# Performance work log

Measured on AMD Instinct MI355X. Metric: run time of the kernel, lower is better.

The kernel has to match this reference:

```python
import jax, jax.numpy as jnp
import numpy as np

N_HEAD = 16
N_EMBD = 2048
HEAD_DIM = N_EMBD // N_HEAD


def setup_inputs() -> dict:
    key = jax.random.key(0)
    kx, kqkv, kp = jax.random.split(key, 3)
    B, S = 2, 2048
    x = jax.random.normal(kx, (B, S, N_EMBD), dtype=jnp.float32)
    # torch nn.Linear weights, stored as [out, in]; y = x @ W.T
    scale = 1.0 / np.sqrt(N_EMBD)
    Wqkv = jax.random.uniform(kqkv, (3 * N_EMBD, N_EMBD), dtype=jnp.float32, minval=-scale, maxval=scale)
    Wproj = jax.random.uniform(kp, (N_EMBD, N_EMBD), dtype=jnp.float32, minval=-scale, maxval=scale)
    return {"x": x, "Wqkv": Wqkv, "Wproj": Wproj}


def reference(x, Wqkv, Wproj):
    B, S, E = x.shape
    qkv = x @ Wqkv.T  # [B,S,3E]
    q, k, v = jnp.split(qkv, 3, axis=2)
    # [B,H,S,D]
    q = q.reshape(B, S, N_HEAD, HEAD_DIM).transpose(0, 2, 1, 3)
    k = k.reshape(B, S, N_HEAD, HEAD_DIM).transpose(0, 2, 1, 3)
    v = v.reshape(B, S, N_HEAD, HEAD_DIM).transpose(0, 2, 1, 3)
    scores = jnp.einsum('bhqd,bhkd->bhqk', q, k) / jnp.sqrt(jnp.float32(HEAD_DIM))
    causal = jnp.tril(jnp.ones((S, S), dtype=bool))  # [S,S]
    scores = jnp.where(causal[None, None, :, :], scores, -jnp.inf)
    weights = jax.nn.softmax(scores, axis=-1)
    out = jnp.einsum('bhqk,bhkd->bhqd', weights, v)  # [B,H,S,D]
    out = out.transpose(0, 2, 1, 3).reshape(B, S, E)
    return out @ Wproj.T
```

## Files before the change

kernel.cpp:

```cpp
#include <hip/hip_runtime.h>
#include <cstdint>
#include <cstddef>

typedef __bf16 bf16;
typedef __bf16 bf16x8 __attribute__((ext_vector_type(8)));
typedef float  f32x4  __attribute__((ext_vector_type(4)));

static_assert(sizeof(bf16x8) == 16, "bf16x8 must be 16B");

__device__ __forceinline__ void async_copy16(const bf16* g, bf16* l) {
  __builtin_amdgcn_global_load_lds(
      (__attribute__((address_space(1))) void*)(g),
      (__attribute__((address_space(3))) void*)(l),
      16, 0, 0);
}

__global__ __launch_bounds__(256)
void conv_f32_bf16(const float* __restrict__ s, bf16* __restrict__ d) {
  const size_t i = ((size_t)blockIdx.x * 256 + threadIdx.x) * 8;
  const f32x4 a = *(const f32x4*)(s + i);
  const f32x4 b = *(const f32x4*)(s + i + 4);
  bf16x8 o;
#pragma unroll
  for (int e = 0; e < 4; ++e) { o[e] = (bf16)a[e]; o[4 + e] = (bf16)b[e]; }
  *(bf16x8*)(d + i) = o;
}

template<int AMODE, int CMODE>
__global__ __launch_bounds__(256, 2)
void gemm_bt(const bf16* __restrict__ A, const bf16* __restrict__ W,
             float* __restrict__ Crow, bf16* __restrict__ Cq,
             bf16* __restrict__ Ck, bf16* __restrict__ Cvt,
             int M, int N, int K, int nbase) {
  __shared__ bf16 As[128 * 64];
  __shared__ bf16 Ws[128 * 64];

  const int tid  = threadIdx.x;
  const int wave = tid >> 6;
  const int lane = tid & 63;
  const int quad = lane >> 4;
  const int r    = lane & 15;
  const int m0 = blockIdx.y * 128;
  const int n0 = blockIdx.x * 128;
  const int wm = (wave >> 1) * 64;
  const int wn = (wave & 1) * 64;

  const int lrow   = lane >> 3;
  const int gchunk = (lane & 7) ^ lrow;

  f32x4 acc[4][4] = {};

  for (int k0 = 0; k0 < K; k0 += 64) {
    __syncthreads();
    for (int j = 0; j < 4; ++j) {
      const int rbase = (wave * 4 + j) * 8;
      const int rowA  = m0 + rbase + lrow;
      const bf16* aSrc;
      if constexpr (AMODE == 2) {
        const int b = rowA >> 11, s = rowA & 2047;
        aSrc = A + ((size_t)(b * 16 + (k0 >> 7)) * 2048 + s) * 128
                 + (k0 & 127) + gchunk * 8;
      } else {
        aSrc = A + (size_t)rowA * K + k0 + gchunk * 8;
      }
      async_copy16(aSrc, As + rbase * 64);
      async_copy16(W + (size_t)(n0 + rbase + lrow) * K + k0 + gchunk * 8,
                   Ws + rbase * 64);
    }
    __syncthreads();
    for (int ks = 0; ks < 2; ++ks) {
      bf16x8 af[4], bfv[4];
      for (int i = 0; i < 4; ++i) {
        const int ar = wm + i * 16 + r;
        af[i]  = *(const bf16x8*)(As + ar * 64 + (((ks * 4 + quad) ^ (ar & 7)) * 8));
        const int br = wn + i * 16 + r;
        bfv[i] = *(const bf16x8*)(Ws + br * 64 + (((ks * 4 + quad) ^ (br & 7)) * 8));
      }
      for (int i = 0; i < 4; ++i)
        for (int j = 0; j < 4; ++j)
          acc[i][j] = __builtin_amdgcn_mfma_f32_16x16x32_bf16(af[i], bfv[j], acc[i][j], 0, 0, 0);
    }
  }

  for (int i = 0; i < 4; ++i) {
    const int growb = m0 + wm + i * 16 + quad * 4;
    for (int j = 0; j < 4; ++j) {
      const int gcol = n0 + wn + j * 16 + r;
      for (int rg = 0; rg < 4; ++rg) {
        const int grow = growb + rg;
        if constexpr (CMODE == 1) {
          const int gc = nbase + gcol;
          const int which = gc >> 11;
          const int h = (gc >> 7) & 15;
          const int d = gc & 127;
          const int b = grow >> 11;
          const int s = grow & 2047;
          const bf16 v = (bf16)acc[i][j][rg];
          if (which == 0)
            Cq[(((size_t)b * 16 + h) * 2048 + s) * 128 + d] = v;
          else if (which == 1)
            Ck[(((size_t)b * 16 + h) * 2048 + s) * 128 + d] = v;
          else
            Cvt[(((size_t)b * 16 + h) * 128 + d) * 2048 + s] = v;
        } else {
          Crow[(size_t)grow * N + gcol] = acc[i][j][rg];
        }
      }
    }
  }
}

__global__ __launch_bounds__(256, 2)
void attn_kernel(bf16* __restrict__ Q, const bf16* __restrict__ K,
                 const bf16* __restrict__ Vt, int S) {
  __shared__ bf16 k_lds[2][64 * 128];
  __shared__ bf16 v_lds[2][128 * 64];
  __shared__ bf16 p_lds[4][32 * 64];

  const int tid = threadIdx.x, wave = tid >> 6, lane = tid & 63;
  const int quad = lane >> 4, r = lane & 15;
  const int bh = blockIdx.y;
  bf16* Qh = Q + (size_t)bh * S * 128;
  const bf16* Kh = K + (size_t)bh * S * 128;
  const bf16* Vth = Vt + (size_t)bh * 128 * S;

  const float sc = 0.0883883476483184f * 1.4426950408889634f;

  auto issue_stage = [&](int kv0, int buf) {
#pragma unroll
    for (int j = 0; j < 4; ++j) {
      const int lin0 = j * 256 + wave * 64;
      const int lin = lin0 + lane;
      const int row = lin >> 4, ch = lin & 15;
      async_copy16(Kh + (size_t)(kv0 + row) * 128 + ((ch ^ (row & 7)) << 3),
                   &k_lds[buf][0] + lin0 * 8);
    }
#pragma unroll
    for (int j = 0; j < 4; ++j) {
      const int lin0 = j * 256 + wave * 64;
      const int lin = lin0 + lane;
      const int row = lin >> 3, c = lin & 7;
      async_copy16(Vth + (size_t)row * S + kv0 + ((c ^ (row & 7)) << 3),
                   &v_lds[buf][0] + lin0 * 8);
    }
  };

  for (int pass = 0; pass < 2; ++pass) {
    const int qb = pass ? blockIdx.x : (15 - blockIdx.x);
    const int q0 = qb << 7;
    const int qrow0 = q0 + wave * 32;
    const int nkv = (q0 + 128) >> 6;

    bf16x8 qf[2][4];
    for (int mt = 0; mt < 2; ++mt)
      for (int ks = 0; ks < 4; ++ks)
        qf[mt][ks] = *(const bf16x8*)(Qh + (size_t)(qrow0 + mt * 16 + r) * 128 + ks * 32 + quad * 8);

    f32x4 o_acc[2][8] = {};
    f32x4 m_run[2], l_run[2];
    for (int mt = 0; mt < 2; ++mt)
      for (int t = 0; t < 4; ++t) { m_run[mt][t] = -1e30f; l_run[mt][t] = 0.f; }

    issue_stage(0, 0);

    for (int kt = 0; kt < nkv; ++kt) {
      const int kv0 = kt << 6;
      const int cur = kt & 1;
      if (kt + 1 < nkv) {
        issue_stage((kt + 1) << 6, cur ^ 1);
        asm volatile("s_waitcnt vmcnt(8)" ::: "memory");
      } else {
        asm volatile("s_waitcnt vmcnt(0)" ::: "memory");
      }
      __builtin_amdgcn_sched_barrier(0);
      __syncthreads();

      if (kv0 <= qrow0 + 31) {
        f32x4 sa[2][4] = {};
        __builtin_amdgcn_s_setprio(1);
        for (int ks = 0; ks < 4; ++ks) {
          bf16x8 kf[4];
          for (int nt = 0; nt < 4; ++nt) {
            const int kr = nt * 16 + r;
            kf[nt] = *(const bf16x8*)(&k_lds[cur][0] + kr * 128 + (((ks * 4 + quad) ^ (kr & 7)) << 3));
          }
          for (int mt = 0; mt < 2; ++mt)
            for (int nt = 0; nt < 4; ++nt)
              sa[mt][nt] = __builtin_amdgcn_mfma_f32_16x16x32_bf16(qf[mt][ks], kf[nt], sa[mt][nt], 0, 0, 0);
        }
        __builtin_amdgcn_s_setprio(0);
        if (kv0 + 63 > qrow0) {
          for (int mt = 0; mt < 2; ++mt)
            for (int nt = 0; nt < 4; ++nt) {
              const int col  = kv0 + nt * 16 + r;
              const int rowb = qrow0 + mt * 16 + quad * 4;
              for (int rg = 0; rg < 4; ++rg)
                if (col > rowb + rg) sa[mt][nt][rg] = -1e30f;
            }
        }
        for (int mt = 0; mt < 2; ++mt) {
          f32x4 mx = sa[mt][0];
          for (int nt = 1; nt < 4; ++nt)
            for (int rg = 0; rg < 4; ++rg) mx[rg] = fmaxf(mx[rg], sa[mt][nt][rg]);
          for (int off = 1; off < 16; off <<= 1)
            for (int rg = 0; rg < 4; ++rg) mx[rg] = fmaxf(mx[rg], __shfl_xor(mx[rg], off, 64));
          float need = mx[0] - m_run[mt][0];
          for (int rg = 1; rg < 4; ++rg) need = fmaxf(need, mx[rg] - m_run[mt][rg]);
          if (need * sc > 8.0f) {
            f32x4 alpha;
            for (int rg = 0; rg < 4; ++rg) {
              const float mnew = fmaxf(m_run[mt][rg], mx[rg]);
              alpha[rg] = exp2f((m_run[mt][rg] - mnew) * sc);
              m_run[mt][rg] = mnew;
              l_run[mt][rg] *= alpha[rg];
            }
            for (int nt2 = 0; nt2 < 8; ++nt2)
              for (int rg = 0; rg < 4; ++rg) o_acc[mt][nt2][rg] *= alpha[rg];
          }
          f32x4 rsum = {0.f, 0.f, 0.f, 0.f};
          for (int nt = 0; nt < 4; ++nt)
            for (int rg = 0; rg < 4; ++rg) {
              const float p = exp2f((sa[mt][nt][rg] - m_run[mt][rg]) * sc);
              sa[mt][nt][rg] = p;
              rsum[rg] += p;
            }
          for (int off = 1; off < 16; off <<= 1)
            for (int rg = 0; rg < 4; ++rg) rsum[rg] += __shfl_xor(rsum[rg], off, 64);
          for (int rg = 0; rg < 4; ++rg) l_run[mt][rg] += rsum[rg];
          for (int nt = 0; nt < 4; ++nt)
            for (int rg = 0; rg < 4; ++rg) {
              const int prow = mt * 16 + quad * 4 + rg;
              const int pcol = nt * 16 + r;
              p_lds[wave][prow * 64 + (((pcol >> 3) ^ (prow & 7)) * 8) + (pcol & 7)] =
                  (bf16)sa[mt][nt][rg];
            }
        }
        __builtin_amdgcn_s_setprio(1);
        for (int ks2 = 0; ks2 < 2; ++ks2) {
          bf16x8 pf[2];
          for (int mt = 0; mt < 2; ++mt) {
            const int prow = mt * 16 + r;
            pf[mt] = *(const bf16x8*)(p_lds[wave] + prow * 64 + (((ks2 * 4 + quad) ^ (prow & 7)) * 8));
          }
          for (int nt2 = 0; nt2 < 8; ++nt2) {
            const int vrow = nt2 * 16 + r;
            const bf16x8 vf = *(const bf16x8*)(&v_lds[cur][0] + vrow * 64 + (((ks2 * 4 + quad) ^ (vrow & 7)) * 8));
            for (int mt = 0; mt < 2; ++mt)
              o_acc[mt][nt2] = __builtin_amdgcn_mfma_f32_16x16x32_bf16(pf[mt], vf, o_acc[mt][nt2], 0, 0, 0);
          }
        }
        __builtin_amdgcn_s_setprio(0);
      }
      __syncthreads();
    }

    for (int mt = 0; mt < 2; ++mt) {
      f32x4 inv;
      for (int rg = 0; rg < 4; ++rg) inv[rg] = 1.0f / l_run[mt][rg];
      for (int nt2 = 0; nt2 < 8; ++nt2) {
        const int d = nt2 * 16 + r;
        for (int rg = 0; rg < 4; ++rg) {
          const int s = qrow0 + mt * 16 + quad * 4 + rg;
          Qh[(size_t)s * 128 + d] = (bf16)(o_acc[mt][nt2][rg] * inv[rg]);
        }
      }
    }
  }
}

extern "C" void kernel_launch(void* const* d_in, const int* in_sizes, int n_in,
                              void* d_out, int out_size, void* d_ws, size_t ws_size,
                              hipStream_t stream) {
  const float* x     = (const float*)d_in[0];
  const float* Wqkv  = (const float*)d_in[1];
  const float* Wproj = (const float*)d_in[2];
  float* out = (float*)d_out;

  const int Bm = 4096, E = 2048;
  const size_t plane = 8388608;

  bf16* qw  = (bf16*)d_ws;
  bf16* vtw = qw + plane;
  bf16* xb  = vtw + plane;
  bf16* kw  = (bf16*)d_out;
  bf16* wqb = kw + plane;

  conv_f32_bf16<<<8388608 / 2048, 256, 0, stream>>>(x, xb);
  conv_f32_bf16<<<6291456 / 2048, 256, 0, stream>>>(Wqkv, wqb);
  gemm_bt<0, 1><<<dim3(3072 / 128, Bm / 128), 256, 0, stream>>>(
      xb, wqb, nullptr, qw, kw, vtw, Bm, 3072, E, 0);
  conv_f32_bf16<<<6291456 / 2048, 256, 0, stream>>>(Wqkv + 6291456, wqb);
  gemm_bt<0, 1><<<dim3(3072 / 128, Bm / 128), 256, 0, stream>>>(
      xb, wqb, nullptr, qw, kw, vtw, Bm, 3072, E, 3072);
  attn_kernel<<<dim3(8, 32), 256, 0, stream>>>(qw, kw, vtw, 2048);
  conv_f32_bf16<<<4194304 / 2048, 256, 0, stream>>>(Wproj, xb);
  gemm_bt<2, 0><<<dim3(2048 / 128, Bm / 128), 256, 0, stream>>>(
      qw, xb, out, nullptr, nullptr, nullptr, Bm, 2048, E, 0);
}
```

Measured before the change: 436.0 us.

## Split attention work across eight waves with sixteen query rows each

```diff
diff --git a/kernel.cpp b/kernel.cpp
--- a/kernel.cpp
+++ b/kernel.cpp
@@ -110,12 +110,12 @@
   }
 }
 
-__global__ __launch_bounds__(256, 2)
+__global__ __launch_bounds__(512, 2)
 void attn_kernel(bf16* __restrict__ Q, const bf16* __restrict__ K,
                  const bf16* __restrict__ Vt, int S) {
   __shared__ bf16 k_lds[2][64 * 128];
   __shared__ bf16 v_lds[2][128 * 64];
-  __shared__ bf16 p_lds[4][32 * 64];
+  __shared__ bf16 p_lds[8][16 * 64];
 
   const int tid = threadIdx.x, wave = tid >> 6, lane = tid & 63;
   const int quad = lane >> 4, r = lane & 15;
@@ -128,16 +128,16 @@
 
   auto issue_stage = [&](int kv0, int buf) {
 #pragma unroll
-    for (int j = 0; j < 4; ++j) {
-      const int lin0 = j * 256 + wave * 64;
+    for (int j = 0; j < 2; ++j) {
+      const int lin0 = j * 512 + wave * 64;
       const int lin = lin0 + lane;
       const int row = lin >> 4, ch = lin & 15;
       async_copy16(Kh + (size_t)(kv0 + row) * 128 + ((ch ^ (row & 7)) << 3),
                    &k_lds[buf][0] + lin0 * 8);
     }
 #pragma unroll
-    for (int j = 0; j < 4; ++j) {
-      const int lin0 = j * 256 + wave * 64;
+    for (int j = 0; j < 2; ++j) {
+      const int lin0 = j * 512 + wave * 64;
       const int lin = lin0 + lane;
       const int row = lin >> 3, c = lin & 7;
       async_copy16(Vth + (size_t)row * S + kv0 + ((c ^ (row & 7)) << 3),
@@ -148,18 +148,16 @@
   for (int pass = 0; pass < 2; ++pass) {
     const int qb = pass ? blockIdx.x : (15 - blockIdx.x);
     const int q0 = qb << 7;
-    const int qrow0 = q0 + wave * 32;
+    const int qrow0 = q0 + wave * 16;
     const int nkv = (q0 + 128) >> 6;
 
-    bf16x8 qf[2][4];
-    for (int mt = 0; mt < 2; ++mt)
-      for (int ks = 0; ks < 4; ++ks)
-        qf[mt][ks] = *(const bf16x8*)(Qh + (size_t)(qrow0 + mt * 16 + r) * 128 + ks * 32 + quad * 8);
-
-    f32x4 o_acc[2][8] = {};
-    f32x4 m_run[2], l_run[2];
-    for (int mt = 0; mt < 2; ++mt)
-      for (int t = 0; t < 4; ++t) { m_run[mt][t] = -1e30f; l_run[mt][t] = 0.f; }
+    bf16x8 qf[4];
+    for (int ks = 0; ks < 4; ++ks)
+      qf[ks] = *(const bf16x8*)(Qh + (size_t)(qrow0 + r) * 128 + ks * 32 + quad * 8);
+
+    f32x4 o_acc[8] = {};
+    f32x4 m_run, l_run;
+    for (int t = 0; t < 4; ++t) { m_run[t] = -1e30f; l_run[t] = 0.f; }
 
     issue_stage(0, 0);
 
@@ -168,15 +166,15 @@
       const int cur = kt & 1;
       if (kt + 1 < nkv) {
         issue_stage((kt + 1) << 6, cur ^ 1);
-        asm volatile("s_waitcnt vmcnt(8)" ::: "memory");
+        asm volatile("s_waitcnt vmcnt(4)" ::: "memory");
       } else {
         asm volatile("s_waitcnt vmcnt(0)" ::: "memory");
       }
       __builtin_amdgcn_sched_barrier(0);
       __syncthreads();
 
-      if (kv0 <= qrow0 + 31) {
-        f32x4 sa[2][4] = {};
+      if (kv0 <= qrow0 + 15) {
+        f32x4 sa[4] = {};
         __builtin_amdgcn_s_setprio(1);
         for (int ks = 0; ks < 4; ++ks) {
           bf16x8 kf[4];
@@ -184,69 +182,61 @@
             const int kr = nt * 16 + r;
             kf[nt] = *(const bf16x8*)(&k_lds[cur][0] + kr * 128 + (((ks * 4 + quad) ^ (kr & 7)) << 3));
           }
-          for (int mt = 0; mt < 2; ++mt)
-            for (int nt = 0; nt < 4; ++nt)
-              sa[mt][nt] = __builtin_amdgcn_mfma_f32_16x16x32_bf16(qf[mt][ks], kf[nt], sa[mt][nt], 0, 0, 0);
+          for (int nt = 0; nt < 4; ++nt)
+            sa[nt] = __builtin_amdgcn_mfma_f32_16x16x32_bf16(qf[ks], kf[nt], sa[nt], 0, 0, 0);
         }
         __builtin_amdgcn_s_setprio(0);
         if (kv0 + 63 > qrow0) {
-          for (int mt = 0; mt < 2; ++mt)
-            for (int nt = 0; nt < 4; ++nt) {
-              const int col  = kv0 + nt * 16 + r;
-              const int rowb = qrow0 + mt * 16 + quad * 4;
-              for (int rg = 0; rg < 4; ++rg)
-                if (col > rowb + rg) sa[mt][nt][rg] = -1e30f;
-            }
-        }
-        for (int mt = 0; mt < 2; ++mt) {
-          f32x4 mx = sa[mt][0];
-          for (int nt = 1; nt < 4; ++nt)
-            for (int rg = 0; rg < 4; ++rg) mx[rg] = fmaxf(mx[rg], sa[mt][nt][rg]);
-          for (int off = 1; off < 16; off <<= 1)
-            for (int rg = 0; rg < 4; ++rg) mx[rg] = fmaxf(mx[rg], __shfl_xor(mx[rg], off, 64));
-          float need = mx[0] - m_run[mt][0];
-          for (int rg = 1; rg < 4; ++rg) need = fmaxf(need, mx[rg] - m_run[mt][rg]);
-          if (need * sc > 8.0f) {
-            f32x4 alpha;
-            for (int rg = 0; rg < 4; ++rg) {
-              const float mnew = fmaxf(m_run[mt][rg], mx[rg]);
-              alpha[rg] = exp2f((m_run[mt][rg] - mnew) * sc);
-              m_run[mt][rg] = mnew;
-              l_run[mt][rg] *= alpha[rg];
-            }
-            for (int nt2 = 0; nt2 < 8; ++nt2)
-              for (int rg = 0; rg < 4; ++rg) o_acc[mt][nt2][rg] *= alpha[rg];
-          }
-          f32x4 rsum = {0.f, 0.f, 0.f, 0.f};
-          for (int nt = 0; nt < 4; ++nt)
-            for (int rg = 0; rg < 4; ++rg) {
-              const float p = exp2f((sa[mt][nt][rg] - m_run[mt][rg]) * sc);
-              sa[mt][nt][rg] = p;
-              rsum[rg] += p;
-            }
-          for (int off = 1; off < 16; off <<= 1)
-            for (int rg = 0; rg < 4; ++rg) rsum[rg] += __shfl_xor(rsum[rg], off, 64);
-          for (int rg = 0; rg < 4; ++rg) l_run[mt][rg] += rsum[rg];
-          for (int nt = 0; nt < 4; ++nt)
-            for (int rg = 0; rg < 4; ++rg) {
-              const int prow = mt * 16 + quad * 4 + rg;
-              const int pcol = nt * 16 + r;
-              p_lds[wave][prow * 64 + (((pcol >> 3) ^ (prow & 7)) * 8) + (pcol & 7)] =
-                  (bf16)sa[mt][nt][rg];
-            }
-        }
+          for (int nt = 0; nt < 4; ++nt) {
+            const int col  = kv0 + nt * 16 + r;
+            const int rowb = qrow0 + quad * 4;
+            for (int rg = 0; rg < 4; ++rg)
+              if (col > rowb + rg) sa[nt][rg] = -1e30f;
+          }
+        }
+        f32x4 mx = sa[0];
+        for (int nt = 1; nt < 4; ++nt)
+          for (int rg = 0; rg < 4; ++rg) mx[rg] = fmaxf(mx[rg], sa[nt][rg]);
+        for (int off = 1; off < 16; off <<= 1)
+          for (int rg = 0; rg < 4; ++rg) mx[rg] = fmaxf(mx[rg], __shfl_xor(mx[rg], off, 64));
+        float need = mx[0] - m_run[0];
+        for (int rg = 1; rg < 4; ++rg) need = fmaxf(need, mx[rg] - m_run[rg]);
+        if (need * sc > 8.0f) {
+          f32x4 alpha;
+          for (int rg = 0; rg < 4; ++rg) {
+            const float mnew = fmaxf(m_run[rg], mx[rg]);
+            alpha[rg] = exp2f((m_run[rg] - mnew) * sc);
+            m_run[rg] = mnew;
+            l_run[rg] *= alpha[rg];
+          }
+          for (int nt2 = 0; nt2 < 8; ++nt2)
+            for (int rg = 0; rg < 4; ++rg) o_acc[nt2][rg] *= alpha[rg];
+        }
+        f32x4 rsum = {0.f, 0.f, 0.f, 0.f};
+        for (int nt = 0; nt < 4; ++nt)
+          for (int rg = 0; rg < 4; ++rg) {
+            const float p = exp2f((sa[nt][rg] - m_run[rg]) * sc);
+            sa[nt][rg] = p;
+            rsum[rg] += p;
+          }
+        for (int off = 1; off < 16; off <<= 1)
+          for (int rg = 0; rg < 4; ++rg) rsum[rg] += __shfl_xor(rsum[rg], off, 64);
+        for (int rg = 0; rg < 4; ++rg) l_run[rg] += rsum[rg];
+        for (int nt = 0; nt < 4; ++nt)
+          for (int rg = 0; rg < 4; ++rg) {
+            const int prow = quad * 4 + rg;
+            const int pcol = nt * 16 + r;
+            p_lds[wave][prow * 64 + (((pcol >> 3) ^ (prow & 7)) * 8) + (pcol & 7)] =
+                (bf16)sa[nt][rg];
+          }
         __builtin_amdgcn_s_setprio(1);
         for (int ks2 = 0; ks2 < 2; ++ks2) {
-          bf16x8 pf[2];
-          for (int mt = 0; mt < 2; ++mt) {
-            const int prow = mt * 16 + r;
-            pf[mt] = *(const bf16x8*)(p_lds[wave] + prow * 64 + (((ks2 * 4 + quad) ^ (prow & 7)) * 8));
-          }
+          const int prow = r;
+          const bf16x8 pf = *(const bf16x8*)(p_lds[wave] + prow * 64 + (((ks2 * 4 + quad) ^ (prow & 7)) * 8));
           for (int nt2 = 0; nt2 < 8; ++nt2) {
             const int vrow = nt2 * 16 + r;
             const bf16x8 vf = *(const bf16x8*)(&v_lds[cur][0] + vrow * 64 + (((ks2 * 4 + quad) ^ (vrow & 7)) * 8));
-            for (int mt = 0; mt < 2; ++mt)
-              o_acc[mt][nt2] = __builtin_amdgcn_mfma_f32_16x16x32_bf16(pf[mt], vf, o_acc[mt][nt2], 0, 0, 0);
+            o_acc[nt2] = __builtin_amdgcn_mfma_f32_16x16x32_bf16(pf, vf, o_acc[nt2], 0, 0, 0);
           }
         }
         __builtin_amdgcn_s_setprio(0);
@@ -254,15 +244,13 @@
       __syncthreads();
     }
 
-    for (int mt = 0; mt < 2; ++mt) {
-      f32x4 inv;
-      for (int rg = 0; rg < 4; ++rg) inv[rg] = 1.0f / l_run[mt][rg];
-      for (int nt2 = 0; nt2 < 8; ++nt2) {
-        const int d = nt2 * 16 + r;
-        for (int rg = 0; rg < 4; ++rg) {
-          const int s = qrow0 + mt * 16 + quad * 4 + rg;
-          Qh[(size_t)s * 128 + d] = (bf16)(o_acc[mt][nt2][rg] * inv[rg]);
-        }
+    f32x4 inv;
+    for (int rg = 0; rg < 4; ++rg) inv[rg] = 1.0f / l_run[rg];
+    for (int nt2 = 0; nt2 < 8; ++nt2) {
+      const int d = nt2 * 16 + r;
+      for (int rg = 0; rg < 4; ++rg) {
+        const int s = qrow0 + quad * 4 + rg;
+        Qh[(size_t)s * 128 + d] = (bf16)(o_acc[nt2][rg] * inv[rg]);
       }
     }
   }
@@ -292,7 +280,7 @@
   conv_f32_bf16<<<6291456 / 2048, 256, 0, stream>>>(Wqkv + 6291456, wqb);
   gemm_bt<0, 1><<<dim3(3072 / 128, Bm / 128), 256, 0, stream>>>(
       xb, wqb, nullptr, qw, kw, vtw, Bm, 3072, E, 3072);
-  attn_kernel<<<dim3(8, 32), 256, 0, stream>>>(qw, kw, vtw, 2048);
+  attn_kernel<<<dim3(8, 32), 512, 0, stream>>>(qw, kw, vtw, 2048);
   conv_f32_bf16<<<4194304 / 2048, 256, 0, stream>>>(Wproj, xb);
   gemm_bt<2, 0><<<dim3(2048 / 128, Bm / 128), 256, 0, stream>>>(
       qw, xb, out, nullptr, nullptr, nullptr, Bm, 2048, E, 0);
```

After: 412.5 us. -5.4%, faster.
